# Optimization experiments

Measured on AMD Instinct MI355X. Metric: run time of the kernel, lower is better.

The kernel has to match this reference:

```python
import jax, jax.numpy as jnp
import numpy as np

BS, D, S, K = 32, 64, 2048, 1024  # batch, embedding_dim, seq_len, num_embeddings


def setup_inputs() -> dict:
    key = jax.random.key(0)
    k1, k2 = jax.random.split(key)
    x = jax.random.normal(k1, (BS, D, S), dtype=jnp.float32)
    # xavier_uniform on [D, K]
    bound = float(np.sqrt(6.0 / (D + K)))
    embeddings = jax.random.uniform(k2, (D, K), dtype=jnp.float32, minval=-bound, maxval=bound)
    return {"x": x, "embeddings": embeddings}


def reference(x, embeddings):
    bs, d, s = x.shape
    k = embeddings.shape[1]
    # [bs, d, s] -> [bs*s, d]
    flat = x.transpose(0, 2, 1).reshape(-1, d)
    unquantized = flat
    # squared distance ||a||^2 - 2 a.b + ||b||^2 -> [N, K]
    a2 = jnp.sum(flat * flat, axis=1, keepdims=True)
    ab2 = 2.0 * (flat @ embeddings)
    b2 = jnp.sum(embeddings * embeddings, axis=0, keepdims=True)
    distance = a2 - ab2 + b2
    encoding_indices = jnp.argmin(distance, axis=1)  # == (-distance).argmax(1)
    one_hot = jax.nn.one_hot(encoding_indices, k, dtype=jnp.int32)  # F.one_hot -> int
    quantized = jnp.take(embeddings.T, encoding_indices, axis=0)  # [N, d] gather
    quantized = quantized.reshape(bs, s, d).transpose(0, 2, 1)  # [bs, d, s]
    e_latent_loss = jnp.mean(jnp.square(quantized - jax.lax.stop_gradient(x)))
    q_latent_loss = jnp.mean(jnp.square(jax.lax.stop_gradient(quantized) - x))
    loss = q_latent_loss + e_latent_loss
    # straight-through estimator
    quantized_st = x + jax.lax.stop_gradient(quantized - x)
    return (
        quantized_st,
        loss,
        one_hot.reshape(bs, s, k).transpose(0, 2, 1),
        encoding_indices.reshape(bs, s),
        distance.reshape(bs, s, k).transpose(0, 2, 1),
        unquantized,
        embeddings.T,
    )
```

## Files before the change

### kernel.cpp

```cpp
#include <hip/hip_runtime.h>

#define BSZ 32
#define DIM 64
#define SEQ 2048
#define KE  1024
#define KC  128
#define ST  128

#define O0 0ull
#define O1 4194304ull
#define O2 4194305ull
#define O3 71303169ull
#define O4 71368705ull
#define O5 138477569ull
#define O6 142671873ull

__global__ __launch_bounds__(256) void vq_prep(const float* __restrict__ E,
                                               float* __restrict__ out,
                                               float* __restrict__ et_ws,
                                               float* __restrict__ b2_ws) {
    __shared__ float T[64][65];
    const int tid  = threadIdx.x;
    const int lane = tid & 63;
    const int sub  = tid >> 6;
    const int k0   = blockIdx.x * 64;
    for (int dd = 0; dd < 16; ++dd) {
        int d = dd * 4 + sub;
        T[d][lane] = E[(size_t)d * KE + k0 + lane];
    }
    __syncthreads();
    for (int ii = 0; ii < 16; ++ii) {
        int kl = ii * 4 + sub;
        float v = T[lane][kl];
        out[O6 + (size_t)(k0 + kl) * 64 + lane] = v;
        et_ws[(size_t)(k0 + kl) * 64 + lane]    = v;
    }
    if (tid < 64) {
        float s = 0.f;
        #pragma unroll
        for (int d = 0; d < 64; ++d) {
            float v = T[d][tid];
            s = fmaf(v, v, s);
        }
        b2_ws[k0 + tid] = s;
    }
    if (blockIdx.x == 0 && tid == 0) out[O1] = 0.f;
}

__global__ __launch_bounds__(256, 2) void vq_main(const float* __restrict__ x,
                                                  const float* __restrict__ E,
                                                  const float* __restrict__ et,
                                                  const float* __restrict__ b2,
                                                  float* __restrict__ out) {
    __shared__ __align__(16) float xt[64][ST];
    __shared__ __align__(16) union UU {
        float e[64][KC];
        struct { float D[16][ST]; int Kk[16][ST]; } red;
        float qt[64][ST];
    } u;
    __shared__ __align__(16) float a2s[ST];

    const int tid = threadIdx.x;
    const int tx  = tid & 15;
    const int ky  = tid >> 4;
    const int b   = blockIdx.x >> 4;
    const int s0  = (blockIdx.x & 15) << 7;

    {
        const float* xb = x + ((size_t)b << 17) + s0;
        #pragma unroll
        for (int i = 0; i < 8; ++i) {
            int f  = (i << 8) + tid;
            int d  = f >> 5;
            int sc = (f & 31) << 2;
            *(float4*)&xt[d][sc] = *(const float4*)(xb + ((size_t)d << 11) + sc);
        }
    }
    __syncthreads();
    if (tid < ST) {
        float s = 0.f;
        #pragma unroll
        for (int d = 0; d < 64; ++d) s = fmaf(xt[d][tid], xt[d][tid], s);
        a2s[tid] = s;
    }

    float bD[8];
    int   bK[8];
    #pragma unroll
    for (int j = 0; j < 8; ++j) { bD[j] = 3.4e38f; bK[j] = 0; }

    float* outD = out + O4 + ((size_t)b << 21) + s0;
    float* outH = out + O2 + ((size_t)b << 21) + s0;

    for (int c = 0; c < KE / KC; ++c) {
        const int kc = c << 7;
        __syncthreads();
        {
            const float* eb = E + kc;
            #pragma unroll
            for (int i = 0; i < 8; ++i) {
                int f  = (i << 8) + tid;
                int d  = f >> 5;
                int kk = (f & 31) << 2;
                *(float4*)&u.e[d][kk] = *(const float4*)(eb + (size_t)d * KE + kk);
            }
        }
        __syncthreads();

        float acc[8][8];
        #pragma unroll
        for (int jk = 0; jk < 8; ++jk)
            #pragma unroll
            for (int js = 0; js < 8; ++js) acc[jk][js] = 0.f;

        #pragma unroll 2
        for (int d = 0; d < 64; ++d) {
            float4 xa  = *(const float4*)&xt[d][tx * 8];
            float4 xb4 = *(const float4*)&xt[d][tx * 8 + 4];
            float4 ea  = *(const float4*)&u.e[d][ky * 8];
            float4 eb4 = *(const float4*)&u.e[d][ky * 8 + 4];
            float xs[8] = {xa.x, xa.y, xa.z, xa.w, xb4.x, xb4.y, xb4.z, xb4.w};
            float es[8] = {ea.x, ea.y, ea.z, ea.w, eb4.x, eb4.y, eb4.z, eb4.w};
            #pragma unroll
            for (int jk = 0; jk < 8; ++jk)
                #pragma unroll
                for (int js = 0; js < 8; ++js)
                    acc[jk][js] = fmaf(es[jk], xs[js], acc[jk][js]);
        }

        {
            float4 b2a = *(const float4*)(b2 + kc + ky * 8);
            float4 b2b = *(const float4*)(b2 + kc + ky * 8 + 4);
            float b2v[8] = {b2a.x, b2a.y, b2a.z, b2a.w, b2b.x, b2b.y, b2b.z, b2b.w};
            float4 av1 = *(const float4*)&a2s[tx * 8];
            float4 av2 = *(const float4*)&a2s[tx * 8 + 4];
            float a2v[8] = {av1.x, av1.y, av1.z, av1.w, av2.x, av2.y, av2.z, av2.w};
            #pragma unroll
            for (int jk = 0; jk < 8; ++jk) {
                const int k = kc + ky * 8 + jk;
                #pragma unroll
                for (int js = 0; js < 8; ++js) {
                    float dist = fmaf(-2.f, acc[jk][js], a2v[js] + b2v[jk]);
                    acc[jk][js] = dist;
                    if (dist < bD[js]) { bD[js] = dist; bK[js] = k; }
                }
            }
        }

        #pragma unroll
        for (int h = 0; h < 2; ++h) {
            __syncthreads();
            if ((ky >> 3) == h) {
                const int r0 = (ky & 7) * 8;
                #pragma unroll
                for (int jk = 0; jk < 8; ++jk) {
                    float4 lo = {acc[jk][0], acc[jk][1], acc[jk][2], acc[jk][3]};
                    float4 hi = {acc[jk][4], acc[jk][5], acc[jk][6], acc[jk][7]};
                    *(float4*)&u.e[r0 + jk][tx * 8]     = lo;
                    *(float4*)&u.e[r0 + jk][tx * 8 + 4] = hi;
                }
            }
            __syncthreads();
            const int kb = kc + (h << 6);
            const float* st = (const float*)u.e;
            #pragma unroll
            for (int i = 0; i < 32; ++i) {
                int f   = (i << 8) + tid;
                int row = f >> 7;
                int sc  = f & 127;
                size_t off = ((size_t)(kb + row) << 11) + sc;
                outD[off] = st[f];
                outH[off] = 0.f;
            }
        }
    }

    __syncthreads();
    #pragma unroll
    for (int js = 0; js < 8; ++js) {
        u.red.D[ky][tx * 8 + js]  = bD[js];
        u.red.Kk[ky][tx * 8 + js] = bK[js];
    }
    __syncthreads();

    if (tid < ST) {
        float bDr = u.red.D[0][tid];
        int   bKr = u.red.Kk[0][tid];
        #pragma unroll
        for (int w = 1; w < 16; ++w) {
            float dw = u.red.D[w][tid];
            int   kw = u.red.Kk[w][tid];
            if (dw < bDr || (dw == bDr && kw < bKr)) { bDr = dw; bKr = kw; }
        }
        out[O3 + (size_t)b * SEQ + s0 + tid] = (float)bKr;
        out[O2 + ((size_t)b << 21) + ((size_t)bKr << 11) + s0 + tid] = 1.f;

        const float* q = et + ((size_t)bKr << 6);
        float lsum = 0.f;
        #pragma unroll
        for (int i = 0; i < 16; ++i) {
            float4 q4 = ((const float4*)q)[i];
            float qs[4] = {q4.x, q4.y, q4.z, q4.w};
            #pragma unroll
            for (int j = 0; j < 4; ++j) {
                int d = i * 4 + j;
                u.qt[d][tid] = qs[j];
                float df = qs[j] - xt[d][tid];
                lsum = fmaf(df, df, lsum);
            }
        }
        #pragma unroll
        for (int m = 32; m >= 1; m >>= 1) lsum += __shfl_xor(lsum, m, 64);
        if ((tid & 63) == 0) atomicAdd(out + O1, lsum * (2.f / 4194304.f));
    }
    __syncthreads();

    {
        float* oq = out + ((size_t)b << 17) + s0;
        #pragma unroll
        for (int i = 0; i < 8; ++i) {
            int f  = (i << 8) + tid;
            int d  = f >> 5;
            int sc = (f & 31) << 2;
            *(float4*)(oq + ((size_t)d << 11) + sc) = *(const float4*)&u.qt[d][sc];
        }
    }
}

__global__ __launch_bounds__(256) void vq_unq(const float* __restrict__ x,
                                              float* __restrict__ out) {
    __shared__ float T[64][65];
    const int tid  = threadIdx.x;
    const int lane = tid & 63;
    const int sub  = tid >> 6;
    const int b    = blockIdx.x >> 5;
    const int s0   = (blockIdx.x & 31) << 6;
    const float* xp = x + ((size_t)b << 17) + s0;
    for (int dd = 0; dd < 16; ++dd) {
        int d = dd * 4 + sub;
        T[d][lane] = xp[((size_t)d << 11) + lane];
    }
    __syncthreads();
    float* op = out + O5 + (((size_t)b << 11) + s0) * 64;
    for (int ii = 0; ii < 16; ++ii) {
        int sl = ii * 4 + sub;
        op[(size_t)sl * 64 + lane] = T[lane][sl];
    }
}

extern "C" void kernel_launch(void* const* d_in, const int* in_sizes, int n_in,
                              void* d_out, int out_size, void* d_ws, size_t ws_size,
                              hipStream_t stream) {
    const float* x = (const float*)d_in[0];
    const float* E = (const float*)d_in[1];
    float* out   = (float*)d_out;
    float* et_ws = (float*)d_ws;
    float* b2_ws = et_ws + 65536;
    vq_prep<<<16, 256, 0, stream>>>(E, out, et_ws, b2_ws);
    vq_main<<<512, 256, 0, stream>>>(x, E, et_ws, b2_ws, out);
    vq_unq<<<1024, 256, 0, stream>>>(x, out);
}
```

Before: 237.9 us.

## Prefetch codebook chunks into registers and swizzle LDS layout for conflict-free reads

Result: slower. 250.9 us (+5.4%).

```diff
diff --git a/kernel.cpp b/kernel.cpp
--- a/kernel.cpp
+++ b/kernel.cpp
@@ -14,6 +14,16 @@
 #define O4 71368705ull
 #define O5 138477569ull
 #define O6 142671873ull
+
+__device__ __forceinline__ void lds_barrier() {
+    asm volatile("s_waitcnt lgkmcnt(0)" ::: "memory");
+    __builtin_amdgcn_s_barrier();
+}
+
+__device__ __forceinline__ int swz(int j) {
+    int t = j >> 1;
+    return ((j & 1) << 6) + ((t & 7) << 2) + ((t >> 3) << 5);
+}
 
 __global__ __launch_bounds__(256) void vq_prep(const float* __restrict__ E,
                                                float* __restrict__ out,
@@ -52,11 +62,11 @@
                                                   const float* __restrict__ et,
                                                   const float* __restrict__ b2,
                                                   float* __restrict__ out) {
-    __shared__ __align__(16) float xt[64][ST];
+    __shared__ __align__(16) float xt[64 * ST];
     __shared__ __align__(16) union UU {
-        float e[64][KC];
+        float e[64 * KC];
         struct { float D[16][ST]; int Kk[16][ST]; } red;
-        float qt[64][ST];
+        float qt[64 * ST];
     } u;
     __shared__ __align__(16) float a2s[ST];
 
@@ -66,22 +76,34 @@
     const int b   = blockIdx.x >> 4;
     const int s0  = (blockIdx.x & 15) << 7;
 
+    float4 er[8];
+    #pragma unroll
+    for (int i = 0; i < 8; ++i) {
+        int f = (i << 8) + tid;
+        int d = f >> 5, j = f & 31;
+        er[i] = *(const float4*)(E + (size_t)d * KE + (j << 2));
+    }
+
     {
         const float* xb = x + ((size_t)b << 17) + s0;
         #pragma unroll
         for (int i = 0; i < 8; ++i) {
-            int f  = (i << 8) + tid;
-            int d  = f >> 5;
-            int sc = (f & 31) << 2;
-            *(float4*)&xt[d][sc] = *(const float4*)(xb + ((size_t)d << 11) + sc);
+            int f = (i << 8) + tid;
+            int d = f >> 5, j = f & 31;
+            float4 v = *(const float4*)(xb + ((size_t)d << 11) + (j << 2));
+            *(float4*)&xt[d * ST + swz(j)] = v;
         }
     }
     __syncthreads();
     if (tid < ST) {
-        float s = 0.f;
-        #pragma unroll
-        for (int d = 0; d < 64; ++d) s = fmaf(xt[d][tid], xt[d][tid], s);
-        a2s[tid] = s;
+        const int wi = swz(tid >> 2) + (tid & 3);
+        float sacc = 0.f;
+        #pragma unroll
+        for (int d = 0; d < 64; ++d) {
+            float v = xt[d * ST + wi];
+            sacc = fmaf(v, v, sacc);
+        }
+        a2s[tid] = sacc;
     }
 
     float bD[8];
@@ -92,20 +114,28 @@
     float* outD = out + O4 + ((size_t)b << 21) + s0;
     float* outH = out + O2 + ((size_t)b << 21) + s0;
 
+    const int xw1 = ((tx & 7) << 2) + ((tx >> 3) << 5);
+    const int ew1 = ((ky & 7) << 2) + ((ky >> 3) << 5);
+
+    #pragma unroll 1
     for (int c = 0; c < KE / KC; ++c) {
         const int kc = c << 7;
-        __syncthreads();
-        {
-            const float* eb = E + kc;
+        lds_barrier();
+        #pragma unroll
+        for (int i = 0; i < 8; ++i) {
+            int f = (i << 8) + tid;
+            int d = f >> 5, j = f & 31;
+            *(float4*)&u.e[d * KC + swz(j)] = er[i];
+        }
+        lds_barrier();
+        if (c < KE / KC - 1) {
             #pragma unroll
             for (int i = 0; i < 8; ++i) {
-                int f  = (i << 8) + tid;
-                int d  = f >> 5;
-                int kk = (f & 31) << 2;
-                *(float4*)&u.e[d][kk] = *(const float4*)(eb + (size_t)d * KE + kk);
-            }
-        }
-        __syncthreads();
+                int f = (i << 8) + tid;
+                int d = f >> 5, j = f & 31;
+                er[i] = *(const float4*)(E + (size_t)d * KE + (kc + KC) + (j << 2));
+            }
+        }
 
         float acc[8][8];
         #pragma unroll
@@ -115,10 +145,10 @@
 
         #pragma unroll 2
         for (int d = 0; d < 64; ++d) {
-            float4 xa  = *(const float4*)&xt[d][tx * 8];
-            float4 xb4 = *(const float4*)&xt[d][tx * 8 + 4];
-            float4 ea  = *(const float4*)&u.e[d][ky * 8];
-            float4 eb4 = *(const float4*)&u.e[d][ky * 8 + 4];
+            float4 xa  = *(const float4*)&xt[d * ST + xw1];
+            float4 xb4 = *(const float4*)&xt[d * ST + xw1 + 64];
+            float4 ea  = *(const float4*)&u.e[d * KC + ew1];
+            float4 eb4 = *(const float4*)&u.e[d * KC + ew1 + 64];
             float xs[8] = {xa.x, xa.y, xa.z, xa.w, xb4.x, xb4.y, xb4.z, xb4.w};
             float es[8] = {ea.x, ea.y, ea.z, ea.w, eb4.x, eb4.y, eb4.z, eb4.w};
             #pragma unroll
@@ -149,33 +179,33 @@
 
         #pragma unroll
         for (int h = 0; h < 2; ++h) {
-            __syncthreads();
+            lds_barrier();
             if ((ky >> 3) == h) {
-                const int r0 = (ky & 7) * 8;
+                const int r0 = (ky & 7) << 3;
                 #pragma unroll
                 for (int jk = 0; jk < 8; ++jk) {
                     float4 lo = {acc[jk][0], acc[jk][1], acc[jk][2], acc[jk][3]};
                     float4 hi = {acc[jk][4], acc[jk][5], acc[jk][6], acc[jk][7]};
-                    *(float4*)&u.e[r0 + jk][tx * 8]     = lo;
-                    *(float4*)&u.e[r0 + jk][tx * 8 + 4] = hi;
+                    *(float4*)&u.e[(r0 + jk) * ST + tx * 8]     = lo;
+                    *(float4*)&u.e[(r0 + jk) * ST + tx * 8 + 4] = hi;
                 }
             }
-            __syncthreads();
+            lds_barrier();
             const int kb = kc + (h << 6);
-            const float* st = (const float*)u.e;
             #pragma unroll
             for (int i = 0; i < 32; ++i) {
                 int f   = (i << 8) + tid;
                 int row = f >> 7;
                 int sc  = f & 127;
                 size_t off = ((size_t)(kb + row) << 11) + sc;
-                outD[off] = st[f];
+                float v = u.e[f];
+                outD[off] = v;
                 outH[off] = 0.f;
             }
         }
     }
 
-    __syncthreads();
+    lds_barrier();
     #pragma unroll
     for (int js = 0; js < 8; ++js) {
         u.red.D[ky][tx * 8 + js]  = bD[js];
@@ -196,6 +226,7 @@
         out[O2 + ((size_t)b << 21) + ((size_t)bKr << 11) + s0 + tid] = 1.f;
 
         const float* q = et + ((size_t)bKr << 6);
+        const int wi = swz(tid >> 2) + (tid & 3);
         float lsum = 0.f;
         #pragma unroll
         for (int i = 0; i < 16; ++i) {
@@ -204,8 +235,8 @@
             #pragma unroll
             for (int j = 0; j < 4; ++j) {
                 int d = i * 4 + j;
-                u.qt[d][tid] = qs[j];
-                float df = qs[j] - xt[d][tid];
+                u.qt[d * ST + tid] = qs[j];
+                float df = qs[j] - xt[d * ST + wi];
                 lsum = fmaf(df, df, lsum);
             }
         }
@@ -222,7 +253,7 @@
             int f  = (i << 8) + tid;
             int d  = f >> 5;
             int sc = (f & 31) << 2;
-            *(float4*)(oq + ((size_t)d << 11) + sc) = *(const float4*)&u.qt[d][sc];
+            *(float4*)(oq + ((size_t)d << 11) + sc) = *(const float4*)&u.qt[d * ST + sc];
         }
     }
 }
```
